# Kernel optimization log

Hardware: AMD Instinct MI355X
Metric: run time of the kernel (lower is better)

## Reference

```python
import jax, jax.numpy as jnp
import numpy as np

B, T, C, H = 32, 512, 256, 8
DEG = 16
EPS = 1e-5


def setup_inputs() -> dict:
    rs = np.random.RandomState(0)
    counts = rs.randint(384, 513, size=B)  # ragged graph sizes, max 512 = T
    N = int(counts.sum())
    E = N * DEG
    # dense-batch scatter indices: node i of graph b -> slot b*T + rank
    idx = np.concatenate([b * T + np.arange(c) for b, c in enumerate(counts)]).astype(np.int64)
    mask = np.zeros((B, T), dtype=bool)
    for b, c in enumerate(counts):
        mask[b, :c] = True
    key = jax.random.key(0)
    ks = jax.random.split(key, 12)
    w = lambda k, shape: jax.random.normal(k, shape, jnp.float32) * 0.02
    z = lambda n: jnp.zeros((n,), jnp.float32)
    o = lambda n: jnp.ones((n,), jnp.float32)
    return dict(
        x=jax.random.normal(ks[0], (N, C), jnp.float32),
        edge_index=jax.random.randint(ks[1], (2, E), 0, N),
        idx=jnp.asarray(idx), mask=jnp.asarray(mask),
        W_root=w(ks[2], (C, C)), W_nbr=w(ks[3], (C, C)), b_conv=z(C),
        Wq=w(ks[4], (C, C)), Wk=w(ks[5], (C, C)), Wv=w(ks[6], (C, C)),
        bq=z(C), bk=z(C), bv=z(C), Wo=w(ks[7], (C, C)), bo=z(C),
        W1=w(ks[8], (C, 2 * C)), b1=z(2 * C), W2=w(ks[9], (2 * C, C)), b2=z(C),
        g1=o(C), be1=z(C), g2=o(C), be2=z(C), g3=o(C), be3=z(C),
    )


def _bn(h, g, b):
    # BatchNorm1d over nodes (training-mode batch stats, biased variance)
    m = h.mean(0)
    v = h.var(0)
    return g * (h - m) * jax.lax.rsqrt(v + EPS) + b


def _forward(x, W_root, W_nbr, b_conv, Wq, Wk, Wv, bq, bk, bv, Wo, bo,
             W1, b1, W2, b2, g1, be1, g2, be2, g3, be3,
             edge_index, idx, mask):
    N = x.shape[0]
    # --- local MPNN (GraphConv): x_i W_root + (sum_{j->i} x_j) W_nbr + b ---
    agg = jax.ops.segment_sum(x[edge_index[0]], edge_index[1], num_segments=N)
    h_local = x @ W_root + agg @ W_nbr + b_conv
    h_local = _bn(h_local + x, g1, be1)  # dropout p=0, residual, norm1
    # --- to_dense_batch: scatter ragged nodes into [B, T, C] ---
    xd = jnp.zeros((B * T, C), x.dtype).at[idx].set(x).reshape(B, T, C)
    # --- global MHA with key_padding_mask = ~mask ---
    Dh = C // H
    q = (xd @ Wq + bq).reshape(B, T, H, Dh)
    k = (xd @ Wk + bk).reshape(B, T, H, Dh)
    v = (xd @ Wv + bv).reshape(B, T, H, Dh)
    scores = jnp.einsum('bqhd,bkhd->bhqk', q, k) * (1.0 / float(np.sqrt(Dh)))
    scores = jnp.where(mask[:, None, None, :], scores, -1e9)
    attn = jax.nn.softmax(scores, axis=-1)
    o = jnp.einsum('bhqk,bkhd->bqhd', attn, v).reshape(B, T, C)
    o = o @ Wo + bo
    # --- unpad (index_select on flattened mask) + residual + norm2 ---
    h_attn = o.reshape(B * T, C)[idx] + x
    h_attn = _bn(h_attn, g2, be2)
    # --- combine branches, MLP with residual, norm3 ---
    out = h_local + h_attn
    out = out + jax.nn.relu(out @ W1 + b1) @ W2 + b2
    return _bn(out, g3, be3)


def reference(x, edge_index, idx, mask, W_root, W_nbr, b_conv, Wq, Wk, Wv,
              bq, bk, bv, Wo, bo, W1, b1, W2, b2,
              g1, be1, g2, be2, g3, be3):
    return _forward(x, W_root, W_nbr, b_conv, Wq, Wk, Wv, bq, bk, bv, Wo, bo,
                    W1, b1, W2, b2, g1, be1, g2, be2, g3, be3,
                    edge_index, idx, mask)
```

## Files before the change

kernel.cpp:

```cpp
#include <hip/hip_runtime.h>
#include <hip/hip_bf16.h>
#include <math.h>

#define Bc 32
#define Tc 512
#define Cc 256
#define Hc 8
#define BT (Bc * Tc)
#define EPS 1e-5f
#define LDAP 40

typedef __bf16 bf16x8 __attribute__((ext_vector_type(8)));
typedef float f32x4 __attribute__((ext_vector_type(4)));
typedef unsigned short us8_t __attribute__((ext_vector_type(8)));

__device__ inline unsigned short f2bf(float f) {
    unsigned int u = __float_as_uint(f);
    u += 0x7fffu + ((u >> 16) & 1u);
    return (unsigned short)(u >> 16);
}
__device__ inline unsigned short f2bf_fast(float f) {
    __bf16 h = (__bf16)f;
    return __builtin_bit_cast(unsigned short, h);
}
__device__ inline float bf2f(unsigned short u) {
    return __uint_as_float((unsigned int)u << 16);
}

__global__ void wcvt_fused_kernel(const float* __restrict__ Wr, const float* __restrict__ Wn,
                                  const float* __restrict__ Wq, const float* __restrict__ Wk,
                                  const float* __restrict__ Wv, const float* __restrict__ Wo,
                                  const float* __restrict__ W1, const float* __restrict__ W2,
                                  const float* __restrict__ bq, const float* __restrict__ bk,
                                  const float* __restrict__ bv,
                                  unsigned short* __restrict__ wsq, float* __restrict__ bqkv,
                                  const float* __restrict__ x, const int* __restrict__ idx,
                                  unsigned short* __restrict__ x_bf,
                                  unsigned short* __restrict__ xd_bf,
                                  const int* __restrict__ ei, int* __restrict__ deg,
                                  int* __restrict__ bcnt, int N, int E) {
    const float scale = 0.17677669529663687f;
    int gid = blockIdx.x * 256 + threadIdx.x;
    const int X0 = 656128 + N * 32;
    if (gid >= X0 + 64) {
        int e = gid - (X0 + 64);
        if (e < E) atomicAdd(&deg[ei[E + e]], 1);
        return;
    }
    if (gid >= X0) {
        int b = gid - X0;
        if (b >= 32) return;
        int lo = 0, hi = N, v0 = b << 9;
        while (lo < hi) { int mid = (lo + hi) >> 1; if (idx[mid] < v0) lo = mid + 1; else hi = mid; }
        int s = lo;
        lo = 0; hi = N; int v1 = (b + 1) << 9;
        while (lo < hi) { int mid = (lo + hi) >> 1; if (idx[mid] < v1) lo = mid + 1; else hi = mid; }
        bcnt[b] = lo - s;
        return;
    }
    if (gid >= 656128) {
        int j = gid - 656128;
        int i = j >> 5;
        if (i >= N) return;
        int c8 = (j & 31) * 8;
        const float* sp = x + (size_t)i * Cc + c8;
        float4 f0 = *(const float4*)sp;
        float4 f1 = *(const float4*)(sp + 4);
        us8_t pk;
        pk[0] = f2bf_fast(f0.x); pk[1] = f2bf_fast(f0.y);
        pk[2] = f2bf_fast(f0.z); pk[3] = f2bf_fast(f0.w);
        pk[4] = f2bf_fast(f1.x); pk[5] = f2bf_fast(f1.y);
        pk[6] = f2bf_fast(f1.z); pk[7] = f2bf_fast(f1.w);
        *(us8_t*)&x_bf[(size_t)i * Cc + c8] = pk;
        int slot = idx[i];
        *(us8_t*)&xd_bf[(size_t)slot * Cc + c8] = pk;
        return;
    }
    if (gid >= 655360) {
        int j = gid - 655360;
        bqkv[j] = (j < 256) ? bq[j] * scale : (j < 512 ? bk[j - 256] : bv[j - 512]);
        return;
    }
    const float* src; int base, K, N_; float mul = 1.f;
    if (gid < 65536)       { src = Wr; base = 0;      K = 256; N_ = 256; }
    else if (gid < 131072) { src = Wn; base = 65536;  K = 256; N_ = 256; }
    else if (gid < 196608) { src = Wq; base = 131072; K = 256; N_ = 256; mul = scale; }
    else if (gid < 262144) { src = Wk; base = 196608; K = 256; N_ = 256; }
    else if (gid < 327680) { src = Wv; base = 262144; K = 256; N_ = 256; }
    else if (gid < 393216) { src = Wo; base = 327680; K = 256; N_ = 256; }
    else if (gid < 524288) { src = W1; base = 393216; K = 256; N_ = 512; }
    else                   { src = W2; base = 524288; K = 512; N_ = 256; }
    int loc = gid - base;
    int n = loc / K, k = loc % K;
    wsq[gid] = f2bf(src[(size_t)k * N_ + n] * mul);
}

__global__ void prefix_kernel(const int* __restrict__ deg, int* __restrict__ start, int N) {
    __shared__ int sums[1024];
    int tid = threadIdx.x;
    int per = (N + 1023) / 1024;
    int base = tid * per;
    int s = 0;
    for (int i = 0; i < per; ++i) {
        int g = base + i;
        if (g < N) s += deg[g];
    }
    sums[tid] = s;
    __syncthreads();
    for (int off = 1; off < 1024; off <<= 1) {
        int v = (tid >= off) ? sums[tid - off] : 0;
        __syncthreads();
        sums[tid] += v;
        __syncthreads();
    }
    int run = (tid == 0) ? 0 : sums[tid - 1];
    for (int i = 0; i < per; ++i) {
        int g = base + i;
        if (g < N) { start[g] = run; run += deg[g]; }
    }
}

__global__ void fill_csr_kernel(const int* __restrict__ ei, const int* __restrict__ start,
                                int* __restrict__ cursor, int* __restrict__ csr, int E) {
    int e = blockIdx.x * 256 + threadIdx.x;
    if (e >= E) return;
    int dst = ei[E + e];
    int pos = atomicAdd(&cursor[dst], 1);
    csr[start[dst] + pos] = ei[e];
}

__global__ __launch_bounds__(256) void gather_kernel(const unsigned short* __restrict__ x_bf,
                                                     const int* __restrict__ csr,
                                                     const int* __restrict__ start,
                                                     const int* __restrict__ deg,
                                                     unsigned short* __restrict__ agg_bf,
                                                     int N) {
    int i = blockIdx.x * 4 + (threadIdx.x >> 6);
    if (i >= N) return;
    int l4 = (threadIdx.x & 63) * 4;
    int s0 = start[i];
    int end = s0 + deg[i];
    f32x4 a0 = {0.f, 0.f, 0.f, 0.f}, a1 = a0, a2 = a0, a3 = a0;
    int e = s0;
    for (; e + 4 <= end; e += 4) {
        int i0 = csr[e + 0];
        int i1 = csr[e + 1];
        int i2 = csr[e + 2];
        int i3 = csr[e + 3];
        ushort4 u0 = *(const ushort4*)(x_bf + (size_t)i0 * Cc + l4);
        ushort4 u1 = *(const ushort4*)(x_bf + (size_t)i1 * Cc + l4);
        ushort4 u2 = *(const ushort4*)(x_bf + (size_t)i2 * Cc + l4);
        ushort4 u3 = *(const ushort4*)(x_bf + (size_t)i3 * Cc + l4);
        a0[0] += bf2f(u0.x); a0[1] += bf2f(u0.y); a0[2] += bf2f(u0.z); a0[3] += bf2f(u0.w);
        a1[0] += bf2f(u1.x); a1[1] += bf2f(u1.y); a1[2] += bf2f(u1.z); a1[3] += bf2f(u1.w);
        a2[0] += bf2f(u2.x); a2[1] += bf2f(u2.y); a2[2] += bf2f(u2.z); a2[3] += bf2f(u2.w);
        a3[0] += bf2f(u3.x); a3[1] += bf2f(u3.y); a3[2] += bf2f(u3.z); a3[3] += bf2f(u3.w);
    }
    for (; e < end; ++e) {
        ushort4 u = *(const ushort4*)(x_bf + (size_t)csr[e] * Cc + l4);
        a0[0] += bf2f(u.x); a0[1] += bf2f(u.y); a0[2] += bf2f(u.z); a0[3] += bf2f(u.w);
    }
    f32x4 s = (a0 + a1) + (a2 + a3);
    ushort4 w4;
    w4.x = f2bf_fast(s[0]); w4.y = f2bf_fast(s[1]);
    w4.z = f2bf_fast(s[2]); w4.w = f2bf_fast(s[3]);
    *(ushort4*)&agg_bf[(size_t)i * Cc + l4] = w4;
}

template <bool RELU, bool OUTBF16, bool STATS>
__global__ __launch_bounds__(256) void gemm_mfma_kernel(
    const unsigned short* __restrict__ A, const int* __restrict__ gidx,
    const unsigned short* __restrict__ Bt,
    const unsigned short* __restrict__ A2, const unsigned short* __restrict__ B2t,
    const float* __restrict__ bias, const float* __restrict__ res,
    void* __restrict__ Cout, float* __restrict__ stats, int M, int K, int Nc) {
    __shared__ unsigned short As[128 * LDAP];
    __shared__ unsigned short Bs[64 * LDAP];
    int tid = threadIdx.x;
    int row0 = blockIdx.y * 128;
    int col0 = blockIdx.x * 64;
    int lane = tid & 63;
    int w = tid >> 6;
    int wr = (w >> 1) * 64;
    int wc = (w & 1) * 32;
    int fr = lane & 15;
    int kk = (lane >> 4) * 8;

    f32x4 acc[4][2] = {};

    int npass = (A2 != nullptr) ? 2 : 1;
    for (int pass = 0; pass < npass; ++pass) {
        const unsigned short* Ap = pass ? A2 : A;
        const unsigned short* Bp = pass ? B2t : Bt;
        int r = tid >> 1;
        int kc = (tid & 1) * 16;
        int ar = row0 + r;
        if (ar >= M) ar = M - 1;
        int arr = gidx ? gidx[ar] : ar;
        const unsigned short* abase = Ap + (size_t)arr * K + kc;
        int bc = tid >> 2;
        int bkc = (tid & 3) * 8;
        const unsigned short* bbase = Bp + (size_t)(col0 + bc) * K + bkc;
        for (int k0 = 0; k0 < K; k0 += 32) {
            __syncthreads();
            *(us8_t*)&As[r * LDAP + kc] = *(const us8_t*)(abase + k0);
            *(us8_t*)&As[r * LDAP + kc + 8] = *(const us8_t*)(abase + k0 + 8);
            *(us8_t*)&Bs[bc * LDAP + bkc] = *(const us8_t*)(bbase + k0);
            __syncthreads();
            bf16x8 bf0 = *(bf16x8*)&Bs[(wc + fr) * LDAP + kk];
            bf16x8 bf1 = *(bf16x8*)&Bs[(wc + 16 + fr) * LDAP + kk];
#pragma unroll
            for (int fm = 0; fm < 4; ++fm) {
                bf16x8 af = *(bf16x8*)&As[(wr + fm * 16 + fr) * LDAP + kk];
                acc[fm][0] = __builtin_amdgcn_mfma_f32_16x16x32_bf16(af, bf0, acc[fm][0], 0, 0, 0);
                acc[fm][1] = __builtin_amdgcn_mfma_f32_16x16x32_bf16(af, bf1, acc[fm][1], 0, 0, 0);
            }
        }
    }
    int rq = (lane >> 4) * 4;
    float cs[2] = {0.f, 0.f}, cq[2] = {0.f, 0.f};
#pragma unroll
    for (int fm = 0; fm < 4; ++fm) {
#pragma unroll
        for (int fn = 0; fn < 2; ++fn) {
            int col = col0 + wc + fn * 16 + fr;
#pragma unroll
            for (int i = 0; i < 4; ++i) {
                int row = row0 + wr + fm * 16 + rq + i;
                if (row < M) {
                    float v = acc[fm][fn][i];
                    if (bias) v += bias[col];
                    if (res) v += res[(size_t)row * Nc + col];
                    if (RELU) v = fmaxf(v, 0.f);
                    if (OUTBF16)
                        ((unsigned short*)Cout)[(size_t)row * Nc + col] = f2bf_fast(v);
                    else
                        ((float*)Cout)[(size_t)row * Nc + col] = v;
                    if (STATS) { cs[fn] += v; cq[fn] += v * v; }
                }
            }
        }
    }
    if (STATS) {
#pragma unroll
        for (int fn = 0; fn < 2; ++fn) {
            cs[fn] += __shfl_xor(cs[fn], 16); cs[fn] += __shfl_xor(cs[fn], 32);
            cq[fn] += __shfl_xor(cq[fn], 16); cq[fn] += __shfl_xor(cq[fn], 32);
        }
        if ((lane >> 4) == 0) {
            int col = col0 + wc + fr;
            atomicAdd(&stats[col], cs[0]);
            atomicAdd(&stats[256 + col], cq[0]);
            atomicAdd(&stats[col + 16], cs[1]);
            atomicAdd(&stats[256 + col + 16], cq[1]);
        }
    }
}

__global__ void bn_apply_kernel(const float* __restrict__ in, float* __restrict__ out,
                                const float* __restrict__ g, const float* __restrict__ be,
                                const float* __restrict__ stats, int M) {
    int gid = blockIdx.x * 256 + threadIdx.x;
    if (gid >= M * Cc) return;
    int c = gid & (Cc - 1);
    float invM = 1.f / (float)M;
    float mean = stats[c] * invM;
    float var = stats[Cc + c] * invM - mean * mean;
    float sc = g[c] * rsqrtf(var + EPS);
    out[gid] = (in[gid] - mean) * sc + be[c];
}

__global__ void bn12_apply_kernel(const float* __restrict__ hpre,
                                  const float* __restrict__ hattn,
                                  const float* __restrict__ g1, const float* __restrict__ be1,
                                  const float* __restrict__ g2, const float* __restrict__ be2,
                                  const float* __restrict__ stats,
                                  float* __restrict__ out, unsigned short* __restrict__ out_bf,
                                  int M) {
    int gid = blockIdx.x * 256 + threadIdx.x;
    if (gid >= M * Cc) return;
    int c = gid & (Cc - 1);
    float invM = 1.f / (float)M;
    float mean1 = stats[c] * invM;
    float var1 = stats[Cc + c] * invM - mean1 * mean1;
    float sc1 = g1[c] * rsqrtf(var1 + EPS);
    float mean2 = stats[2 * Cc + c] * invM;
    float var2 = stats[3 * Cc + c] * invM - mean2 * mean2;
    float sc2 = g2[c] * rsqrtf(var2 + EPS);
    float v = (hpre[gid] - mean1) * sc1 + be1[c] + (hattn[gid] - mean2) * sc2 + be2[c];
    out[gid] = v;
    out_bf[gid] = f2bf_fast(v);
}

__global__ __launch_bounds__(256) void attn_mfma_kernel(const unsigned short* __restrict__ qkvb,
                                                        const int* __restrict__ bcnt,
                                                        unsigned short* __restrict__ o_bf) {
    const int blk = ((blockIdx.x & 7) << 7) | ((int)blockIdx.x >> 3);
    const int qt = blk & 3;
    const int bh = blk >> 2;
    const int b = bh >> 3;
    const int h = bh & 7;
    const int tid = threadIdx.x;
    const int lane = tid & 63;
    const int w = tid >> 6;
    const int fr = lane & 15;
    const int g = lane >> 4;
    const int kk = g * 8;
    const int q0 = qt * 128 + w * 32;

    __shared__ unsigned short Ks[32 * LDAP];
    __shared__ unsigned short Vt[32 * LDAP];
    __shared__ unsigned short Pl[4][2][16 * LDAP];

    const int count = bcnt[b];

    const unsigned short* qp = qkvb + (size_t)(b * Tc + q0 + fr) * 768 + h * 32 + kk;
    bf16x8 qa0 = *(const bf16x8*)qp;
    bf16x8 qa1 = *(const bf16x8*)(qp + (size_t)16 * 768);

    f32x4 op00 = {0.f, 0.f, 0.f, 0.f}, op01 = op00;
    f32x4 op10 = op00, op11 = op00;
    float l0 = 0.f, l1 = 0.f;
    float m0 = -1e30f, m1 = -1e30f;

    const int nt = (count + 31) >> 5;
    for (int t = 0; t < nt; ++t) {
        const int kbase = t * 32;
        __syncthreads();
        {
            int key = tid >> 3;
            int d4 = (tid & 7) * 4;
            const unsigned short* kp =
                qkvb + (size_t)(b * Tc + kbase + key) * 768 + 256 + h * 32 + d4;
            *(ushort4*)&Ks[key * LDAP + d4] = *(const ushort4*)kp;
        }
        {
            int vkey = tid & 31;
            int d0 = (tid >> 5) * 4;
            const unsigned short* vp =
                qkvb + (size_t)(b * Tc + kbase + vkey) * 768 + 512 + h * 32 + d0;
            ushort4 vv = *(const ushort4*)vp;
            Vt[(d0 + 0) * LDAP + vkey] = vv.x;
            Vt[(d0 + 1) * LDAP + vkey] = vv.y;
            Vt[(d0 + 2) * LDAP + vkey] = vv.z;
            Vt[(d0 + 3) * LDAP + vkey] = vv.w;
        }
        __syncthreads();

        bf16x8 ka0 = *(bf16x8*)&Ks[fr * LDAP + kk];
        bf16x8 ka1 = *(bf16x8*)&Ks[(16 + fr) * LDAP + kk];
        f32x4 z = {0.f, 0.f, 0.f, 0.f};
        f32x4 s00 = __builtin_amdgcn_mfma_f32_16x16x32_bf16(ka0, qa0, z, 0, 0, 0);
        f32x4 s10 = __builtin_amdgcn_mfma_f32_16x16x32_bf16(ka1, qa0, z, 0, 0, 0);
        f32x4 s01 = __builtin_amdgcn_mfma_f32_16x16x32_bf16(ka0, qa1, z, 0, 0, 0);
        f32x4 s11 = __builtin_amdgcn_mfma_f32_16x16x32_bf16(ka1, qa1, z, 0, 0, 0);

#pragma unroll
        for (int i = 0; i < 4; ++i) {
            bool v0 = (kbase + g * 4 + i) < count;
            bool v1 = (kbase + 16 + g * 4 + i) < count;
            s00[i] = v0 ? s00[i] : -1e30f;
            s01[i] = v0 ? s01[i] : -1e30f;
            s10[i] = v1 ? s10[i] : -1e30f;
            s11[i] = v1 ? s11[i] : -1e30f;
        }

        float r0_ = fmaxf(fmaxf(fmaxf(s00[0], s00[1]), fmaxf(s00[2], s00[3])),
                          fmaxf(fmaxf(s10[0], s10[1]), fmaxf(s10[2], s10[3])));
        r0_ = fmaxf(r0_, __shfl_xor(r0_, 16));
        r0_ = fmaxf(r0_, __shfl_xor(r0_, 32));
        float mn0 = fmaxf(m0, r0_);
        float c0 = __expf(m0 - mn0);
        m0 = mn0;
        l0 *= c0;
        float p00[4], p10[4];
#pragma unroll
        for (int i = 0; i < 4; ++i) {
            p00[i] = __expf(s00[i] - mn0);
            p10[i] = __expf(s10[i] - mn0);
            l0 += p00[i] + p10[i];
        }
        float r1_ = fmaxf(fmaxf(fmaxf(s01[0], s01[1]), fmaxf(s01[2], s01[3])),
                          fmaxf(fmaxf(s11[0], s11[1]), fmaxf(s11[2], s11[3])));
        r1_ = fmaxf(r1_, __shfl_xor(r1_, 16));
        r1_ = fmaxf(r1_, __shfl_xor(r1_, 32));
        float mn1 = fmaxf(m1, r1_);
        float c1 = __expf(m1 - mn1);
        m1 = mn1;
        l1 *= c1;
        float p01[4], p11[4];
#pragma unroll
        for (int i = 0; i < 4; ++i) {
            p01[i] = __expf(s01[i] - mn1);
            p11[i] = __expf(s11[i] - mn1);
            l1 += p01[i] + p11[i];
        }

        unsigned short* pw0 = &Pl[w][0][0];
        unsigned short* pw1 = &Pl[w][1][0];
        ushort4 q00, q10, q01, q11;
        q00.x = f2bf_fast(p00[0]); q00.y = f2bf_fast(p00[1]);
        q00.z = f2bf_fast(p00[2]); q00.w = f2bf_fast(p00[3]);
        q10.x = f2bf_fast(p10[0]); q10.y = f2bf_fast(p10[1]);
        q10.z = f2bf_fast(p10[2]); q10.w = f2bf_fast(p10[3]);
        q01.x = f2bf_fast(p01[0]); q01.y = f2bf_fast(p01[1]);
        q01.z = f2bf_fast(p01[2]); q01.w = f2bf_fast(p01[3]);
        q11.x = f2bf_fast(p11[0]); q11.y = f2bf_fast(p11[1]);
        q11.z = f2bf_fast(p11[2]); q11.w = f2bf_fast(p11[3]);
        *(ushort4*)&pw0[fr * LDAP + g * 4] = q00;
        *(ushort4*)&pw0[fr * LDAP + 16 + g * 4] = q10;
        *(ushort4*)&pw1[fr * LDAP + g * 4] = q01;
        *(ushort4*)&pw1[fr * LDAP + 16 + g * 4] = q11;

#pragma unroll
        for (int i = 0; i < 4; ++i) {
            float ci0 = __shfl(c0, g * 4 + i);
            float ci1 = __shfl(c1, g * 4 + i);
            op00[i] *= ci0; op01[i] *= ci0;
            op10[i] *= ci1; op11[i] *= ci1;
        }

        asm volatile("s_waitcnt lgkmcnt(0)" ::: "memory");
        __builtin_amdgcn_sched_barrier(0);

        bf16x8 pa0 = *(bf16x8*)&pw0[fr * LDAP + kk];
        bf16x8 pa1 = *(bf16x8*)&pw1[fr * LDAP + kk];
        bf16x8 vb0 = *(bf16x8*)&Vt[fr * LDAP + kk];
        bf16x8 vb1 = *(bf16x8*)&Vt[(16 + fr) * LDAP + kk];
        op00 = __builtin_amdgcn_mfma_f32_16x16x32_bf16(pa0, vb0, op00, 0, 0, 0);
        op01 = __builtin_amdgcn_mfma_f32_16x16x32_bf16(pa0, vb1, op01, 0, 0, 0);
        op10 = __builtin_amdgcn_mfma_f32_16x16x32_bf16(pa1, vb0, op10, 0, 0, 0);
        op11 = __builtin_amdgcn_mfma_f32_16x16x32_bf16(pa1, vb1, op11, 0, 0, 0);
    }

    l0 += __shfl_xor(l0, 16); l0 += __shfl_xor(l0, 32);
    l1 += __shfl_xor(l1, 16); l1 += __shfl_xor(l1, 32);
    float inv0 = 1.f / l0;
    float inv1 = 1.f / l1;
#pragma unroll
    for (int i = 0; i < 4; ++i) {
        float li0 = __shfl(inv0, g * 4 + i);
        float li1 = __shfl(inv1, g * 4 + i);
        size_t row0 = (size_t)(b * Tc + q0 + g * 4 + i);
        size_t row1 = row0 + 16;
        o_bf[row0 * Cc + h * 32 + fr] = f2bf_fast(op00[i] * li0);
        o_bf[row0 * Cc + h * 32 + 16 + fr] = f2bf_fast(op01[i] * li0);
        o_bf[row1 * Cc + h * 32 + fr] = f2bf_fast(op10[i] * li1);
        o_bf[row1 * Cc + h * 32 + 16 + fr] = f2bf_fast(op11[i] * li1);
    }
}

extern "C" void kernel_launch(void* const* d_in, const int* in_sizes, int n_in,
                              void* d_out, int out_size, void* d_ws, size_t ws_size,
                              hipStream_t stream) {
    const float* x      = (const float*)d_in[0];
    const int*   ei     = (const int*)d_in[1];
    const int*   idx    = (const int*)d_in[2];
    const float* W_root = (const float*)d_in[4];
    const float* W_nbr  = (const float*)d_in[5];
    const float* b_conv = (const float*)d_in[6];
    const float* Wq     = (const float*)d_in[7];
    const float* Wk     = (const float*)d_in[8];
    const float* Wv     = (const float*)d_in[9];
    const float* bq     = (const float*)d_in[10];
    const float* bk     = (const float*)d_in[11];
    const float* bv     = (const float*)d_in[12];
    const float* Wo     = (const float*)d_in[13];
    const float* bo     = (const float*)d_in[14];
    const float* W1     = (const float*)d_in[15];
    const float* b1     = (const float*)d_in[16];
    const float* W2     = (const float*)d_in[17];
    const float* b2     = (const float*)d_in[18];
    const float* g1     = (const float*)d_in[19];
    const float* be1    = (const float*)d_in[20];
    const float* g2     = (const float*)d_in[21];
    const float* be2    = (const float*)d_in[22];
    const float* g3     = (const float*)d_in[23];
    const float* be3    = (const float*)d_in[24];

    const int N = in_sizes[0] / Cc;
    const int E = in_sizes[1] / 2;

    float* ws = (float*)d_ws;
    float* hB    = ws;
    float* bqkv  = hB + (size_t)N * Cc;
    unsigned short* wsq    = (unsigned short*)(bqkv + 768);
    unsigned short* x_bf   = wsq + 655360;
    unsigned short* hB_bf  = x_bf + (size_t)N * Cc;
    unsigned short* hid_bf = hB_bf + (size_t)N * Cc;
    unsigned short* xd_bf  = hid_bf + (size_t)N * 2 * Cc;
    unsigned short* qkvb   = xd_bf + (size_t)BT * Cc;
    int*   bcnt   = (int*)(qkvb + (size_t)BT * 768);
    float* stats  = (float*)(bcnt + 32);
    int*   deg    = (int*)(stats + 6 * Cc);
    int*   cursor = deg + N;
    int*   csr    = cursor + N;
    int*   startA = csr + E;
    float* bufA   = (float*)d_out;
    unsigned short* agg_bf = (unsigned short*)d_out;
    unsigned short* ao = xd_bf;

    const unsigned short* Wrt   = wsq;
    const unsigned short* Wnt   = wsq + 65536;
    const unsigned short* Wqkvt = wsq + 131072;
    const unsigned short* Wot   = wsq + 327680;
    const unsigned short* W1t   = wsq + 393216;
    const unsigned short* W2t   = wsq + 524288;

    (void)hipMemsetAsync(stats, 0, (6 * Cc) * sizeof(float) + 2 * (size_t)N * sizeof(int), stream);

    {
        int total = 656128 + N * 32 + 64 + E;
        wcvt_fused_kernel<<<(total + 255) / 256, 256, 0, stream>>>(
            W_root, W_nbr, Wq, Wk, Wv, Wo, W1, W2, bq, bk, bv, wsq, bqkv,
            x, idx, x_bf, xd_bf, ei, deg, bcnt, N, E);
    }

    prefix_kernel<<<1, 1024, 0, stream>>>(deg, startA, N);
    fill_csr_kernel<<<(E + 255) / 256, 256, 0, stream>>>(ei, startA, cursor, csr, E);
    gather_kernel<<<(N + 3) / 4, 256, 0, stream>>>(x_bf, csr, startA, deg, agg_bf, N);

    {
        dim3 grid(Cc / 64, (N + 127) / 128);
        gemm_mfma_kernel<false, false, true><<<grid, 256, 0, stream>>>(
            x_bf, nullptr, Wrt, agg_bf, Wnt, b_conv, x, hB, stats, N, Cc, Cc);
    }

    {
        dim3 grid(768 / 64, BT / 128);
        gemm_mfma_kernel<false, true, false><<<grid, 256, 0, stream>>>(
            xd_bf, nullptr, Wqkvt, nullptr, nullptr, bqkv, nullptr, qkvb, nullptr, BT, Cc, 768);
    }

    attn_mfma_kernel<<<Bc * Hc * 4, 256, 0, stream>>>(qkvb, bcnt, ao);

    {
        dim3 grid(Cc / 64, (N + 127) / 128);
        gemm_mfma_kernel<false, false, true><<<grid, 256, 0, stream>>>(
            ao, idx, Wot, nullptr, nullptr, bo, x, bufA, stats + 2 * Cc, N, Cc, Cc);
    }

    bn12_apply_kernel<<<(N * Cc + 255) / 256, 256, 0, stream>>>(
        hB, bufA, g1, be1, g2, be2, stats, hB, hB_bf, N);

    {
        dim3 grid(512 / 64, (N + 127) / 128);
        gemm_mfma_kernel<true, true, false><<<grid, 256, 0, stream>>>(
            hB_bf, nullptr, W1t, nullptr, nullptr, b1, nullptr, hid_bf, nullptr, N, Cc, 512);
    }

    {
        dim3 grid(Cc / 64, (N + 127) / 128);
        gemm_mfma_kernel<false, false, true><<<grid, 256, 0, stream>>>(
            hid_bf, nullptr, W2t, nullptr, nullptr, b2, hB, bufA, stats + 4 * Cc, N, 512, Cc);
    }

    bn_apply_kernel<<<(N * Cc + 255) / 256, 256, 0, stream>>>(
        bufA, bufA, g3, be3, stats + 4 * Cc, N);
}
```

Measured before the change: 264.7 us.

## Replace prefix-sum CSR build with fixed-stride buckets and fuse conv/QKV GEMMs

The in-degree count, the single-block prefix scan and the separate memset are replaced by fixed-stride adjacency buckets of 128 slots per node. These are filled with one atomic cursor per destination, and the cursor count drives the gather. Workspace zeroing moves into the fused conversion kernel. The conv GEMM and the QKV GEMM are merged into one launch that dispatches on block index, cutting launch count and letting both fill the GPU together. Risks: edges are silently dropped for in-degree above 128, and the bucket array needs N*128 ints of workspace, far more than the old CSR.

Result: faster. 226.4 us (-14.5%).

```diff
diff --git a/kernel.cpp b/kernel.cpp
--- a/kernel.cpp
+++ b/kernel.cpp
@@ -9,6 +9,7 @@
 #define BT (Bc * Tc)
 #define EPS 1e-5f
 #define LDAP 40
+#define CSTRIDE 128
 
 typedef __bf16 bf16x8 __attribute__((ext_vector_type(8)));
 typedef float f32x4 __attribute__((ext_vector_type(4)));
@@ -37,14 +38,18 @@
                                   const float* __restrict__ x, const int* __restrict__ idx,
                                   unsigned short* __restrict__ x_bf,
                                   unsigned short* __restrict__ xd_bf,
-                                  const int* __restrict__ ei, int* __restrict__ deg,
-                                  int* __restrict__ bcnt, int N, int E) {
+                                  int* __restrict__ bcnt, int* __restrict__ zbase,
+                                  int N, int nzero4) {
     const float scale = 0.17677669529663687f;
     int gid = blockIdx.x * 256 + threadIdx.x;
     const int X0 = 656128 + N * 32;
-    if (gid >= X0 + 64) {
-        int e = gid - (X0 + 64);
-        if (e < E) atomicAdd(&deg[ei[E + e]], 1);
+    const int XZ = X0 + 64;
+    if (gid >= XZ) {
+        int j = gid - XZ;
+        if (j < nzero4) {
+            int4 z = {0, 0, 0, 0};
+            *(int4*)&zbase[j * 4] = z;
+        }
         return;
     }
     if (gid >= X0) {
@@ -95,58 +100,33 @@
     wsq[gid] = f2bf(src[(size_t)k * N_ + n] * mul);
 }
 
-__global__ void prefix_kernel(const int* __restrict__ deg, int* __restrict__ start, int N) {
-    __shared__ int sums[1024];
-    int tid = threadIdx.x;
-    int per = (N + 1023) / 1024;
-    int base = tid * per;
-    int s = 0;
-    for (int i = 0; i < per; ++i) {
-        int g = base + i;
-        if (g < N) s += deg[g];
-    }
-    sums[tid] = s;
-    __syncthreads();
-    for (int off = 1; off < 1024; off <<= 1) {
-        int v = (tid >= off) ? sums[tid - off] : 0;
-        __syncthreads();
-        sums[tid] += v;
-        __syncthreads();
-    }
-    int run = (tid == 0) ? 0 : sums[tid - 1];
-    for (int i = 0; i < per; ++i) {
-        int g = base + i;
-        if (g < N) { start[g] = run; run += deg[g]; }
-    }
-}
-
-__global__ void fill_csr_kernel(const int* __restrict__ ei, const int* __restrict__ start,
-                                int* __restrict__ cursor, int* __restrict__ csr, int E) {
+__global__ void fill_csr_kernel(const int* __restrict__ ei, int* __restrict__ cursor,
+                                int* __restrict__ csr, int E) {
     int e = blockIdx.x * 256 + threadIdx.x;
     if (e >= E) return;
     int dst = ei[E + e];
     int pos = atomicAdd(&cursor[dst], 1);
-    csr[start[dst] + pos] = ei[e];
+    if (pos < CSTRIDE) csr[(size_t)dst * CSTRIDE + pos] = ei[e];
 }
 
 __global__ __launch_bounds__(256) void gather_kernel(const unsigned short* __restrict__ x_bf,
                                                      const int* __restrict__ csr,
-                                                     const int* __restrict__ start,
-                                                     const int* __restrict__ deg,
+                                                     const int* __restrict__ cursor,
                                                      unsigned short* __restrict__ agg_bf,
                                                      int N) {
     int i = blockIdx.x * 4 + (threadIdx.x >> 6);
     if (i >= N) return;
     int l4 = (threadIdx.x & 63) * 4;
-    int s0 = start[i];
-    int end = s0 + deg[i];
+    int dcount = cursor[i];
+    if (dcount > CSTRIDE) dcount = CSTRIDE;
+    const int* row = csr + (size_t)i * CSTRIDE;
     f32x4 a0 = {0.f, 0.f, 0.f, 0.f}, a1 = a0, a2 = a0, a3 = a0;
-    int e = s0;
-    for (; e + 4 <= end; e += 4) {
-        int i0 = csr[e + 0];
-        int i1 = csr[e + 1];
-        int i2 = csr[e + 2];
-        int i3 = csr[e + 3];
+    int e = 0;
+    for (; e + 4 <= dcount; e += 4) {
+        int i0 = row[e + 0];
+        int i1 = row[e + 1];
+        int i2 = row[e + 2];
+        int i3 = row[e + 3];
         ushort4 u0 = *(const ushort4*)(x_bf + (size_t)i0 * Cc + l4);
         ushort4 u1 = *(const ushort4*)(x_bf + (size_t)i1 * Cc + l4);
         ushort4 u2 = *(const ushort4*)(x_bf + (size_t)i2 * Cc + l4);
@@ -156,8 +136,8 @@
         a2[0] += bf2f(u2.x); a2[1] += bf2f(u2.y); a2[2] += bf2f(u2.z); a2[3] += bf2f(u2.w);
         a3[0] += bf2f(u3.x); a3[1] += bf2f(u3.y); a3[2] += bf2f(u3.z); a3[3] += bf2f(u3.w);
     }
-    for (; e < end; ++e) {
-        ushort4 u = *(const ushort4*)(x_bf + (size_t)csr[e] * Cc + l4);
+    for (; e < dcount; ++e) {
+        ushort4 u = *(const ushort4*)(x_bf + (size_t)row[e] * Cc + l4);
         a0[0] += bf2f(u.x); a0[1] += bf2f(u.y); a0[2] += bf2f(u.z); a0[3] += bf2f(u.w);
     }
     f32x4 s = (a0 + a1) + (a2 + a3);
@@ -168,17 +148,16 @@
 }
 
 template <bool RELU, bool OUTBF16, bool STATS>
-__global__ __launch_bounds__(256) void gemm_mfma_kernel(
+__device__ __forceinline__ void gemm_body(
     const unsigned short* __restrict__ A, const int* __restrict__ gidx,
     const unsigned short* __restrict__ Bt,
     const unsigned short* __restrict__ A2, const unsigned short* __restrict__ B2t,
     const float* __restrict__ bias, const float* __restrict__ res,
-    void* __restrict__ Cout, float* __restrict__ stats, int M, int K, int Nc) {
-    __shared__ unsigned short As[128 * LDAP];
-    __shared__ unsigned short Bs[64 * LDAP];
+    void* __restrict__ Cout, float* __restrict__ stats, int M, int K, int Nc,
+    int bx, int by, unsigned short* As, unsigned short* Bs) {
     int tid = threadIdx.x;
-    int row0 = blockIdx.y * 128;
-    int col0 = blockIdx.x * 64;
+    int row0 = by * 128;
+    int col0 = bx * 64;
     int lane = tid & 63;
     int w = tid >> 6;
     int wr = (w >> 1) * 64;
@@ -254,6 +233,39 @@
             atomicAdd(&stats[col + 16], cs[1]);
             atomicAdd(&stats[256 + col + 16], cq[1]);
         }
+    }
+}
+
+template <bool RELU, bool OUTBF16, bool STATS>
+__global__ __launch_bounds__(256) void gemm_mfma_kernel(
+    const unsigned short* A, const int* gidx, const unsigned short* Bt,
+    const unsigned short* A2, const unsigned short* B2t,
+    const float* bias, const float* res, void* Cout, float* stats,
+    int M, int K, int Nc) {
+    __shared__ unsigned short As[128 * LDAP];
+    __shared__ unsigned short Bs[64 * LDAP];
+    gemm_body<RELU, OUTBF16, STATS>(A, gidx, Bt, A2, B2t, bias, res, Cout, stats,
+                                    M, K, Nc, blockIdx.x, blockIdx.y, As, Bs);
+}
+
+__global__ __launch_bounds__(256) void convqkv_kernel(
+    const unsigned short* __restrict__ x_bf, const unsigned short* __restrict__ agg_bf,
+    const unsigned short* __restrict__ Wrt, const unsigned short* __restrict__ Wnt,
+    const unsigned short* __restrict__ Wqkvt,
+    const float* __restrict__ b_conv, const float* __restrict__ x,
+    float* __restrict__ hB, float* __restrict__ stats,
+    const unsigned short* __restrict__ xd_bf, const float* __restrict__ bqkv,
+    unsigned short* __restrict__ qkvb, int N, int convBlocks) {
+    __shared__ unsigned short As[128 * LDAP];
+    __shared__ unsigned short Bs[64 * LDAP];
+    int blk = blockIdx.x;
+    if (blk < convBlocks) {
+        gemm_body<false, false, true>(x_bf, nullptr, Wrt, agg_bf, Wnt, b_conv, x,
+                                      hB, stats, N, 256, 256, blk & 3, blk >> 2, As, Bs);
+    } else {
+        int q = blk - convBlocks;
+        gemm_body<false, true, false>(xd_bf, nullptr, Wqkvt, nullptr, nullptr, bqkv, nullptr,
+                                      qkvb, nullptr, BT, 256, 768, q % 12, q / 12, As, Bs);
     }
 }
 
@@ -492,10 +504,8 @@
     unsigned short* qkvb   = xd_bf + (size_t)BT * Cc;
     int*   bcnt   = (int*)(qkvb + (size_t)BT * 768);
     float* stats  = (float*)(bcnt + 32);
-    int*   deg    = (int*)(stats + 6 * Cc);
-    int*   cursor = deg + N;
+    int*   cursor = (int*)(stats + 6 * Cc);
     int*   csr    = cursor + N;
-    int*   startA = csr + E;
     float* bufA   = (float*)d_out;
     unsigned short* agg_bf = (unsigned short*)d_out;
     unsigned short* ao = xd_bf;
@@ -507,29 +517,26 @@
     const unsigned short* W1t   = wsq + 393216;
     const unsigned short* W2t   = wsq + 524288;
 
-    (void)hipMemsetAsync(stats, 0, (6 * Cc) * sizeof(float) + 2 * (size_t)N * sizeof(int), stream);
+    const int nzero = 6 * Cc + N;
+    const int nzero4 = (nzero + 3) / 4;
 
     {
-        int total = 656128 + N * 32 + 64 + E;
+        int total = 656128 + N * 32 + 64 + nzero4;
         wcvt_fused_kernel<<<(total + 255) / 256, 256, 0, stream>>>(
             W_root, W_nbr, Wq, Wk, Wv, Wo, W1, W2, bq, bk, bv, wsq, bqkv,
-            x, idx, x_bf, xd_bf, ei, deg, bcnt, N, E);
-    }
-
-    prefix_kernel<<<1, 1024, 0, stream>>>(deg, startA, N);
-    fill_csr_kernel<<<(E + 255) / 256, 256, 0, stream>>>(ei, startA, cursor, csr, E);
-    gather_kernel<<<(N + 3) / 4, 256, 0, stream>>>(x_bf, csr, startA, deg, agg_bf, N);
+            x, idx, x_bf, xd_bf, bcnt, (int*)stats, N, nzero4);
+    }
+
+    fill_csr_kernel<<<(E + 255) / 256, 256, 0, stream>>>(ei, cursor, csr, E);
+
+    gather_kernel<<<(N + 3) / 4, 256, 0, stream>>>(x_bf, csr, cursor, agg_bf, N);
 
     {
-        dim3 grid(Cc / 64, (N + 127) / 128);
-        gemm_mfma_kernel<false, false, true><<<grid, 256, 0, stream>>>(
-            x_bf, nullptr, Wrt, agg_bf, Wnt, b_conv, x, hB, stats, N, Cc, Cc);
-    }
-
-    {
-        dim3 grid(768 / 64, BT / 128);
-        gemm_mfma_kernel<false, true, false><<<grid, 256, 0, stream>>>(
-            xd_bf, nullptr, Wqkvt, nullptr, nullptr, bqkv, nullptr, qkvb, nullptr, BT, Cc, 768);
+        int convBlocks = 4 * ((N + 127) / 128);
+        int qkvBlocks = 12 * (BT / 128);
+        convqkv_kernel<<<convBlocks + qkvBlocks, 256, 0, stream>>>(
+            x_bf, agg_bf, Wrt, Wnt, Wqkvt, b_conv, x, hB, stats,
+            xd_bf, bqkv, qkvb, N, convBlocks);
     }
 
     attn_mfma_kernel<<<Bc * Hc * 4, 256, 0, stream>>>(qkvb, bcnt, ao);
```
